# Optimization experiments

Hardware: AMD Instinct MI355X
Metric: run time of the kernel (lower is better)

The kernel has to match this reference:

```python
import jax, jax.numpy as jnp
import numpy as np

D_MODEL = 512
N_LAYERS = 6
N_HEADS = 8
INNER = 2048
VOCAB = 2048
SEQ = 128
BATCH = 256
HEAD_DIM = D_MODEL // N_HEADS
EPS = 1e-5


def _pos_encoding(seq_len, d_model):
    pos = jnp.arange(seq_len, dtype=jnp.float32)[:, None]          # [S,1]
    i = jnp.arange(d_model // 2, dtype=jnp.float32)[None, :]       # [1,d/2]
    theta = pos / jnp.power(10000.0, 2.0 * i / d_model)            # [S,d/2]
    # interleave sin at even indices, cos at odd indices
    return jnp.stack([jnp.sin(theta), jnp.cos(theta)], axis=-1).reshape(seq_len, d_model)


def _layer_norm_2d(x):
    # F.layer_norm(x, (N, dims)): normalize over last TWO dims, no affine
    m = jnp.mean(x, axis=(1, 2), keepdims=True)
    v = jnp.mean(jnp.square(x - m), axis=(1, 2), keepdims=True)
    return (x - m) / jnp.sqrt(v + EPS)


def setup_inputs() -> dict:
    key = jax.random.key(0)
    ks = jax.random.split(key, 12)
    s = 0.02
    x = jax.random.randint(ks[0], (BATCH, SEQ), 0, VOCAB)
    emb = jax.random.normal(ks[1], (VOCAB, D_MODEL), jnp.float32) * s
    Wq = jax.random.normal(ks[2], (N_LAYERS, N_HEADS, D_MODEL, HEAD_DIM), jnp.float32) * s
    bq = jax.random.normal(ks[3], (N_LAYERS, N_HEADS, HEAD_DIM), jnp.float32) * s
    Wk = jax.random.normal(ks[4], (N_LAYERS, N_HEADS, D_MODEL, HEAD_DIM), jnp.float32) * s
    bk = jax.random.normal(ks[5], (N_LAYERS, N_HEADS, HEAD_DIM), jnp.float32) * s
    Wv = jax.random.normal(ks[6], (N_LAYERS, N_HEADS, D_MODEL, HEAD_DIM), jnp.float32) * s
    bv = jax.random.normal(ks[7], (N_LAYERS, N_HEADS, HEAD_DIM), jnp.float32) * s
    W1 = jax.random.normal(ks[8], (N_LAYERS, D_MODEL, INNER), jnp.float32) * s
    b1 = jax.random.normal(ks[9], (N_LAYERS, INNER), jnp.float32) * s
    W2 = jax.random.normal(ks[10], (N_LAYERS, INNER, D_MODEL), jnp.float32) * s
    b2 = jax.random.normal(ks[11], (N_LAYERS, D_MODEL), jnp.float32) * s
    return {"x": x, "emb": emb, "Wq": Wq, "bq": bq, "Wk": Wk, "bk": bk,
            "Wv": Wv, "bv": bv, "W1": W1, "b1": b1, "W2": W2, "b2": b2}


def reference(x, emb, Wq, bq, Wk, bk, Wv, bv, W1, b1, W2, b2):
    B, S = x.shape
    pe = _pos_encoding(SEQ, D_MODEL)
    h = emb[x] + pe[None, :, :]                                     # [B,S,D]
    scale = HEAD_DIM ** -0.5
    for l in range(N_LAYERS):
        q = jnp.einsum('bsd,hde->bhse', h, Wq[l]) + bq[l][None, :, None, :]
        k = jnp.einsum('bsd,hde->bhse', h, Wk[l]) + bk[l][None, :, None, :]
        v = jnp.einsum('bsd,hde->bhse', h, Wv[l]) + bv[l][None, :, None, :]
        scores = jnp.einsum('bhse,bhte->bhst', q, k) * scale        # no softmax!
        attn = jnp.einsum('bhst,bhte->bhse', scores, v)             # [B,H,S,E]
        attn = jnp.transpose(attn, (0, 2, 1, 3)).reshape(B, S, D_MODEL)
        h = _layer_norm_2d(h + attn)
        ff = jax.nn.relu(h @ W1[l] + b1[l]) @ W2[l] + b2[l]
        h = _layer_norm_2d(h + ff)
    return h
```

## Files before the change

kernel.cpp:

```cpp
#include <hip/hip_runtime.h>
#include <stdint.h>

#define NLAYERS 6
#define DMODEL  512
#define NHEADS  8
#define HDIM    64
#define INNER   2048
#define SEQ     128
#define BATCH   256
#define NTOK    (BATCH*SEQ)

typedef __attribute__((ext_vector_type(4))) float f32x4;
typedef __attribute__((ext_vector_type(8))) _Float16 hfrag;

typedef const __attribute__((address_space(1))) void* gas1p;
typedef __attribute__((address_space(3))) void* las3p;

__device__ __forceinline__ void load_lds16(const void* g, void* l) {
  __builtin_amdgcn_global_load_lds((gas1p)(uintptr_t)g, (las3p)(uint32_t)(uintptr_t)l, 16, 0, 0);
}

__device__ __forceinline__ ushort f2h(float f) {
  return __builtin_bit_cast(ushort, (_Float16)f);
}
__device__ __forceinline__ float h2f(ushort u) {
  return (float)__builtin_bit_cast(_Float16, u);
}

__device__ __forceinline__ f32x4 mfma16(hfrag a, hfrag b, f32x4 c) {
  return __builtin_amdgcn_mfma_f32_16x16x32_f16(a, b, c, 0, 0, 0);
}


__global__ void prep_qkv(const float* __restrict__ Wq, const float* __restrict__ Wk,
                         const float* __restrict__ Wv, const float* __restrict__ bq,
                         const float* __restrict__ bk, const float* __restrict__ bv,
                         ushort* __restrict__ Wt, float* __restrict__ biasq) {
  int idx = blockIdx.x*256 + threadIdx.x;
  if (idx >= NLAYERS*1536*512) return;
  const int k = idx & 511;
  const int n = (idx >> 9) % 1536;
  const int l = idx / (1536*512);
  const int which = n >> 9, hh = (n >> 6) & 7, e = n & 63;
  const float* W = (which == 0) ? Wq : ((which == 1) ? Wk : Wv);
  Wt[idx] = f2h(W[(((size_t)l*NHEADS + hh)*DMODEL + k)*HDIM + e]);
  if (k == 0) {
    const float* bb = (which == 0) ? bq : ((which == 1) ? bk : bv);
    biasq[l*1536 + n] = bb[((size_t)l*NHEADS + hh)*HDIM + e];
  }
}

__global__ void prep_w1(const float* __restrict__ W1, ushort* __restrict__ W1t) {
  int idx = blockIdx.x*256 + threadIdx.x;
  if (idx >= NLAYERS*INNER*512) return;
  const int k = idx & 511;
  const int n = (idx >> 9) % INNER;
  const int l = idx / (INNER*512);
  W1t[idx] = f2h(W1[((size_t)l*DMODEL + k)*INNER + n]);
}

__global__ void prep_w2(const float* __restrict__ W2, ushort* __restrict__ W2t) {
  int idx = blockIdx.x*256 + threadIdx.x;
  if (idx >= NLAYERS*512*INNER) return;
  const int k = idx & 2047;
  const int n = (idx >> 11) & 511;
  const int l = idx / (512*INNER);
  W2t[idx] = f2h(W2[((size_t)l*INNER + k)*DMODEL + n]);
}


__global__ void embed_kernel(const int* __restrict__ x, const float* __restrict__ emb,
                             ushort* __restrict__ hb) {
  const int t = blockIdx.x;
  const int i = threadIdx.x;
  const int s = t & (SEQ-1);
  const int tok = x[t];
  const float freq = expf(-(float)i * (9.210340371976184f / 256.0f));
  const float th = (float)s * freq;
  const float sn = sinf(th), cs = cosf(th);
  const size_t base = (size_t)t*DMODEL;
  const float v0 = emb[(size_t)tok*DMODEL + 2*i]     + sn;
  const float v1 = emb[(size_t)tok*DMODEL + 2*i + 1] + cs;
  *(uint*)(hb + base + 2*i) = (uint)f2h(v0) | ((uint)f2h(v1) << 16);
}


template<int K, int EPI>
__global__ __launch_bounds__(256, 2) void gemm_t(
    const ushort* __restrict__ A, const ushort* __restrict__ Bt,
    const float* __restrict__ bias, ushort* __restrict__ outb,
    const int ldc, const int nbn) {
  __shared__ __align__(16) char lds[73728];
  constexpr int NKT = K / 32;
  const int t = threadIdx.x;
  const int lane = t & 63, wc = t >> 6;
  const int cpx = (int)gridDim.x >> 3;
  const int wg  = ((int)blockIdx.x & 7) * cpx + ((int)blockIdx.x >> 3);
  const int bm = wg / nbn, bn = wg % nbn;

  const int fr = lane & 15;
  const int cxor = (((lane >> 4) ^ ((fr >> 1) & 3)) << 4);

  float bias_r[4];
  #pragma unroll
  for (int n = 0; n < 4; ++n) bias_r[n] = bias[bn*256 + wc*64 + n*16 + fr];
  asm volatile("" : "+v"(bias_r[0]), "+v"(bias_r[1]), "+v"(bias_r[2]), "+v"(bias_r[3]));

  const int srow = t >> 2;
  const int scc  = (t & 3) ^ ((t >> 3) & 3);
  const ushort* aSrc = A  + ((size_t)bm*128 + srow)*K + scc*8;
  const ushort* bSrc = Bt + ((size_t)bn*256 + srow)*K + scc*8;

  auto stage_t = [&](int j, int slot) {
    char* dst = lds + slot*24576 + t*16;
    const ushort* as = aSrc + j*32;
    load_lds16(as,                  dst);
    load_lds16(as + (size_t)64*K,   dst + 4096);
    const ushort* bs = bSrc + j*32;
    #pragma unroll
    for (int i = 0; i < 4; ++i)
      load_lds16(bs + (size_t)(i*64)*K, dst + 8192 + i*4096);
  };

  f32x4 acc[8][4] = {};

  stage_t(0, 0); stage_t(1, 1);
  asm volatile("s_waitcnt vmcnt(6)" ::: "memory");
  __builtin_amdgcn_s_barrier();

  int rs = 0, ss = 2;
  #pragma unroll 1
  for (int kt = 0; kt < NKT; ++kt) {
    const char* sl = lds + rs*24576;
    hfrag a[8], b[4];
    #pragma unroll
    for (int m = 0; m < 8; ++m)
      a[m] = *(const hfrag*)(sl + (m*16 + fr)*64 + cxor);
    #pragma unroll
    for (int n = 0; n < 4; ++n)
      b[n] = *(const hfrag*)(sl + 8192 + (wc*64 + n*16 + fr)*64 + cxor);
    if (kt + 2 < NKT) stage_t(kt + 2, ss);
    __builtin_amdgcn_s_setprio(1);
    #pragma unroll
    for (int m = 0; m < 8; ++m)
      #pragma unroll
      for (int n = 0; n < 4; ++n)
        acc[m][n] = mfma16(a[m], b[n], acc[m][n]);
    __builtin_amdgcn_s_setprio(0);
    if (kt + 2 < NKT) {
      asm volatile("s_waitcnt vmcnt(6)" ::: "memory");
    } else if (kt + 2 == NKT) {
      asm volatile("s_waitcnt vmcnt(0)" ::: "memory");
    }
    if (kt + 1 < NKT) __builtin_amdgcn_s_barrier();
    rs = (rs == 2) ? 0 : rs + 1;
    ss = (ss == 2) ? 0 : ss + 1;
  }

  #pragma unroll
  for (int m = 0; m < 8; ++m) {
    __syncthreads();
    #pragma unroll
    for (int n = 0; n < 4; ++n) {
      const int cc16 = wc*4 + n;
      #pragma unroll
      for (int r4 = 0; r4 < 4; ++r4) {
        const int row = ((lane >> 4) << 2) + r4;
        float v = acc[m][n][r4] + bias_r[n];
        if constexpr (EPI == 1) v = fmaxf(v, 0.0f);
        *(ushort*)(lds + row*512 + ((cc16 ^ (row >> 2)) << 5) + fr*2) = f2h(v);
      }
    }
    __syncthreads();
    const int er = t >> 4;
    ushort* gp = outb + (size_t)(bm*128 + m*16 + er)*ldc + bn*256;
    #pragma unroll
    for (int p = 0; p < 2; ++p) {
      const int cj = (t & 15) + p*16;
      const uint4 v = *(const uint4*)(lds + er*512 + (((cj >> 1) ^ (er >> 2)) << 5) + ((cj & 1) << 4));
      *(uint4*)(gp + cj*8) = v;
    }
  }
}


__global__ __launch_bounds__(512, 1) void attn_ln(
    const ushort* __restrict__ qkv, ushort* __restrict__ hb) {
  __shared__ __align__(16) char lds[131072];
  __shared__ float red_[8], redq_[8], stat_[2];
  const int t = threadIdx.x;
  const int w = t >> 6, lane = t & 63;
  const int b = blockIdx.x, h = w;
  const int fr = lane & 15;
  const ushort* tokbase = qkv + (size_t)b*SEQ*1536;
  ushort* wl  = (ushort*)(lds + w*16384);
  ushort* kch = wl;
  ushort* vch = wl + 2048;

  f32x4 acc1[4][4] = {};
  #pragma unroll 1
  for (int sb = 0; sb < 4; ++sb) {
    const int s0 = sb*32;
    const int sr = lane >> 1;
    #pragma unroll
    for (int i = 0; i < 4; ++i) {
      const int cc  = i*2 + (lane & 1);
      const int ccs = cc ^ (sr & 7);
      const ushort* g = tokbase + (size_t)(s0+sr)*1536 + h*64 + cc*8;
      *(uint4*)(kch + sr*64 + ccs*8) = *(const uint4*)(g + 512);
      *(uint4*)(vch + sr*64 + ccs*8) = *(const uint4*)(g + 1024);
    }
    hfrag ak[4], av[4];
    #pragma unroll
    for (int m = 0; m < 4; ++m) {
      const int e1 = m*16 + (lane & 15);
      const int ccb = e1 >> 3, el = e1 & 7;
      #pragma unroll
      for (int j = 0; j < 8; ++j) {
        const int s = (lane >> 4)*8 + j;
        ak[m][j] = __builtin_bit_cast(_Float16, kch[s*64 + ((ccb ^ (s & 7))*8) + el]);
        av[m][j] = __builtin_bit_cast(_Float16, vch[s*64 + ((ccb ^ (s & 7))*8) + el]);
      }
    }
    #pragma unroll
    for (int m = 0; m < 4; ++m)
      #pragma unroll
      for (int n = 0; n < 4; ++n)
        acc1[m][n] = mfma16(ak[m], av[n], acc1[m][n]);
  }

  ushort* tv = wl;
  #pragma unroll
  for (int m = 0; m < 4; ++m)
    #pragma unroll
    for (int n = 0; n < 4; ++n)
      #pragma unroll
      for (int r4 = 0; r4 < 4; ++r4) {
        const int e1 = m*16 + (lane >> 4)*4 + r4;
        const int e2 = n*16 + (lane & 15);
        tv[e2*72 + e1] = f2h(acc1[m][n][r4] * 0.125f);
      }

  f32x4 acc2[8][4] = {};
  #pragma unroll
  for (int eb = 0; eb < 2; ++eb) {
    const int e1b = eb*32 + (lane >> 4)*8;
    hfrag aq[8], bk2[4];
    #pragma unroll
    for (int m = 0; m < 8; ++m) {
      const int s = m*16 + (lane & 15);
      aq[m] = *(const hfrag*)(tokbase + (size_t)s*1536 + h*64 + e1b);
    }
    #pragma unroll
    for (int n = 0; n < 4; ++n) {
      const int e2 = n*16 + (lane & 15);
      bk2[n] = *(const hfrag*)(tv + e2*72 + e1b);
    }
    #pragma unroll
    for (int m = 0; m < 8; ++m)
      #pragma unroll
      for (int n = 0; n < 4; ++n)
        acc2[m][n] = mfma16(aq[m], bk2[n], acc2[m][n]);
  }

  __syncthreads();
  #pragma unroll
  for (int m = 0; m < 8; ++m)
    #pragma unroll
    for (int n = 0; n < 4; ++n)
      #pragma unroll
      for (int r4 = 0; r4 < 4; ++r4) {
        const int row = m*16 + ((lane >> 4) << 2) + r4;
        const int ch  = (w*4 + n) ^ ((row >> 2) & 3) ^ (w >> 1);
        *(ushort*)(lds + row*1024 + ch*32 + fr*2) = f2h(acc2[m][n][r4]);
      }
  __syncthreads();

  const int r = t >> 2, qd = t & 3;
  const ushort* hrow = hb + ((size_t)b*SEQ + r)*DMODEL + qd*128;
  uint4 vc[16];
  float s = 0.f, q2 = 0.f;
  #pragma unroll
  for (int j = 0; j < 8; ++j) {
    const int ch = (qd*8 + j) ^ ((r >> 2) & 3) ^ qd;
    const uint4 d0 = *(const uint4*)(lds + r*1024 + ch*32);
    const uint4 d1 = *(const uint4*)(lds + r*1024 + ch*32 + 16);
    const uint4 h0 = *(const uint4*)(hrow + j*16);
    const uint4 h1 = *(const uint4*)(hrow + j*16 + 8);
    uint4 v0, v1;
    #pragma unroll
    for (int c = 0; c < 4; ++c) {
      float a0 = h2f((ushort)((&h0.x)[c] & 0xffffu)) + h2f((ushort)((&d0.x)[c] & 0xffffu));
      float a1 = h2f((ushort)((&h0.x)[c] >> 16))     + h2f((ushort)((&d0.x)[c] >> 16));
      float b0 = h2f((ushort)((&h1.x)[c] & 0xffffu)) + h2f((ushort)((&d1.x)[c] & 0xffffu));
      float b1 = h2f((ushort)((&h1.x)[c] >> 16))     + h2f((ushort)((&d1.x)[c] >> 16));
      s += a0 + a1 + b0 + b1;
      q2 += a0*a0 + a1*a1 + b0*b0 + b1*b1;
      (&v0.x)[c] = (uint)f2h(a0) | ((uint)f2h(a1) << 16);
      (&v1.x)[c] = (uint)f2h(b0) | ((uint)f2h(b1) << 16);
    }
    vc[2*j] = v0; vc[2*j+1] = v1;
  }
  #pragma unroll
  for (int off = 32; off > 0; off >>= 1) {
    s  += __shfl_down(s, off);
    q2 += __shfl_down(q2, off);
  }
  if (lane == 0) { red_[w] = s; redq_[w] = q2; }
  __syncthreads();
  if (t == 0) {
    float S = 0.f, Q = 0.f;
    #pragma unroll
    for (int i = 0; i < 8; ++i) { S += red_[i]; Q += redq_[i]; }
    const float mean = S * (1.0f/65536.0f);
    stat_[0] = mean;
    stat_[1] = rsqrtf(Q * (1.0f/65536.0f) - mean*mean + 1e-5f);
  }
  __syncthreads();
  const float mean = stat_[0], rstd = stat_[1];
  ushort* orow = hb + ((size_t)b*SEQ + r)*DMODEL + qd*128;
  #pragma unroll
  for (int j = 0; j < 16; ++j) {
    const uint4 u = vc[j];
    uint4 o;
    #pragma unroll
    for (int c = 0; c < 4; ++c) {
      const float o0 = (h2f((ushort)((&u.x)[c] & 0xffffu)) - mean) * rstd;
      const float o1 = (h2f((ushort)((&u.x)[c] >> 16))     - mean) * rstd;
      (&o.x)[c] = (uint)f2h(o0) | ((uint)f2h(o1) << 16);
    }
    *(uint4*)(orow + j*8) = o;
  }
}


template<bool FINAL>
__global__ __launch_bounds__(512, 1) void gemm_f(
    const ushort* __restrict__ A, const ushort* __restrict__ Bt,
    const float* __restrict__ bias, ushort* __restrict__ hb, float* __restrict__ hf) {
  __shared__ __align__(16) char lds[131072];
  __shared__ float red_[8], redq_[8], stat_[2];
  constexpr int K = 2048, NKT = 64;
  const int t = threadIdx.x;
  const int lane = t & 63, w = t >> 6;
  const int bm = blockIdx.x;
  const int fr = lane & 15;
  const int cxor = (((lane >> 4) ^ ((fr >> 1) & 3)) << 4);

  float bias_r[4];
  #pragma unroll
  for (int n = 0; n < 4; ++n) bias_r[n] = bias[w*64 + n*16 + fr];
  asm volatile("" : "+v"(bias_r[0]), "+v"(bias_r[1]), "+v"(bias_r[2]), "+v"(bias_r[3]));

  const int srow = t >> 2;
  const int scc  = (t & 3) ^ ((t >> 3) & 3);
  const ushort* aSrc = A  + ((size_t)bm*128 + srow)*K + scc*8;
  const ushort* bSrc = Bt + (size_t)srow*K + scc*8;

  auto stage = [&](int j, int slot) {
    char* dst = lds + slot*40960 + t*16;
    load_lds16(aSrc + j*32, dst);
    #pragma unroll
    for (int i = 0; i < 4; ++i)
      load_lds16(bSrc + (size_t)(i*128)*K + j*32, dst + 8192 + i*8192);
  };

  f32x4 acc[8][4] = {};

  stage(0, 0); stage(1, 1);
  asm volatile("s_waitcnt vmcnt(5)" ::: "memory");
  __builtin_amdgcn_s_barrier();

  int rs = 0, ss = 2;
  #pragma unroll 1
  for (int kt = 0; kt < NKT; ++kt) {
    const char* sl = lds + rs*40960;
    hfrag a[8], b[4];
    #pragma unroll
    for (int m = 0; m < 8; ++m)
      a[m] = *(const hfrag*)(sl + (m*16 + fr)*64 + cxor);
    #pragma unroll
    for (int n = 0; n < 4; ++n)
      b[n] = *(const hfrag*)(sl + 8192 + (w*64 + n*16 + fr)*64 + cxor);
    if (kt + 2 < NKT) stage(kt + 2, ss);
    __builtin_amdgcn_s_setprio(1);
    #pragma unroll
    for (int m = 0; m < 8; ++m)
      #pragma unroll
      for (int n = 0; n < 4; ++n)
        acc[m][n] = mfma16(a[m], b[n], acc[m][n]);
    __builtin_amdgcn_s_setprio(0);
    if (kt + 2 < NKT) {
      asm volatile("s_waitcnt vmcnt(5)" ::: "memory");
    } else if (kt + 2 == NKT) {
      asm volatile("s_waitcnt vmcnt(0)" ::: "memory");
    }
    if (kt + 1 < NKT) __builtin_amdgcn_s_barrier();
    rs = (rs == 2) ? 0 : rs + 1;
    ss = (ss == 2) ? 0 : ss + 1;
  }

  __syncthreads();
  #pragma unroll
  for (int m = 0; m < 8; ++m)
    #pragma unroll
    for (int n = 0; n < 4; ++n)
      #pragma unroll
      for (int r4 = 0; r4 < 4; ++r4) {
        const int row = m*16 + ((lane >> 4) << 2) + r4;
        const int ch  = (w*4 + n) ^ ((row >> 2) & 3) ^ (w >> 1);
        *(ushort*)(lds + row*1024 + ch*32 + fr*2) = f2h(acc[m][n][r4] + bias_r[n]);
      }
  __syncthreads();

  const int r = t >> 2, qd = t & 3;
  const ushort* hrow = hb + ((size_t)bm*SEQ + r)*DMODEL + qd*128;
  uint4 vc[16];
  float s = 0.f, q2 = 0.f;
  #pragma unroll
  for (int j = 0; j < 8; ++j) {
    const int ch = (qd*8 + j) ^ ((r >> 2) & 3) ^ qd;
    const uint4 d0 = *(const uint4*)(lds + r*1024 + ch*32);
    const uint4 d1 = *(const uint4*)(lds + r*1024 + ch*32 + 16);
    const uint4 h0 = *(const uint4*)(hrow + j*16);
    const uint4 h1 = *(const uint4*)(hrow + j*16 + 8);
    uint4 v0, v1;
    #pragma unroll
    for (int c = 0; c < 4; ++c) {
      float a0 = h2f((ushort)((&h0.x)[c] & 0xffffu)) + h2f((ushort)((&d0.x)[c] & 0xffffu));
      float a1 = h2f((ushort)((&h0.x)[c] >> 16))     + h2f((ushort)((&d0.x)[c] >> 16));
      float b0 = h2f((ushort)((&h1.x)[c] & 0xffffu)) + h2f((ushort)((&d1.x)[c] & 0xffffu));
      float b1 = h2f((ushort)((&h1.x)[c] >> 16))     + h2f((ushort)((&d1.x)[c] >> 16));
      s += a0 + a1 + b0 + b1;
      q2 += a0*a0 + a1*a1 + b0*b0 + b1*b1;
      (&v0.x)[c] = (uint)f2h(a0) | ((uint)f2h(a1) << 16);
      (&v1.x)[c] = (uint)f2h(b0) | ((uint)f2h(b1) << 16);
    }
    vc[2*j] = v0; vc[2*j+1] = v1;
  }
  #pragma unroll
  for (int off = 32; off > 0; off >>= 1) {
    s  += __shfl_down(s, off);
    q2 += __shfl_down(q2, off);
  }
  if (lane == 0) { red_[w] = s; redq_[w] = q2; }
  __syncthreads();
  if (t == 0) {
    float S = 0.f, Q = 0.f;
    #pragma unroll
    for (int i = 0; i < 8; ++i) { S += red_[i]; Q += redq_[i]; }
    const float mean = S * (1.0f/65536.0f);
    stat_[0] = mean;
    stat_[1] = rsqrtf(Q * (1.0f/65536.0f) - mean*mean + 1e-5f);
  }
  __syncthreads();
  const float mean = stat_[0], rstd = stat_[1];
  if constexpr (FINAL) {
    float* frow = hf + ((size_t)bm*SEQ + r)*DMODEL + qd*128;
    #pragma unroll
    for (int j = 0; j < 16; ++j) {
      const uint4 u = vc[j];
      f32x4 o0, o1;
      #pragma unroll
      for (int c = 0; c < 2; ++c) {
        o0[2*c]   = (h2f((ushort)((&u.x)[c] & 0xffffu)) - mean) * rstd;
        o0[2*c+1] = (h2f((ushort)((&u.x)[c] >> 16))     - mean) * rstd;
        o1[2*c]   = (h2f((ushort)((&u.x)[c+2] & 0xffffu)) - mean) * rstd;
        o1[2*c+1] = (h2f((ushort)((&u.x)[c+2] >> 16))     - mean) * rstd;
      }
      *(f32x4*)(frow + j*8)     = o0;
      *(f32x4*)(frow + j*8 + 4) = o1;
    }
  } else {
    ushort* orow = hb + ((size_t)bm*SEQ + r)*DMODEL + qd*128;
    #pragma unroll
    for (int j = 0; j < 16; ++j) {
      const uint4 u = vc[j];
      uint4 o;
      #pragma unroll
      for (int c = 0; c < 4; ++c) {
        const float o0 = (h2f((ushort)((&u.x)[c] & 0xffffu)) - mean) * rstd;
        const float o1 = (h2f((ushort)((&u.x)[c] >> 16))     - mean) * rstd;
        (&o.x)[c] = (uint)f2h(o0) | ((uint)f2h(o1) << 16);
      }
      *(uint4*)(orow + j*8) = o;
    }
  }
}


extern "C" void kernel_launch(void* const* d_in, const int* in_sizes, int n_in,
                              void* d_out, int out_size, void* d_ws, size_t ws_size,
                              hipStream_t stream) {
  const int*   x   = (const int*)d_in[0];
  const float* emb = (const float*)d_in[1];
  const float* Wq  = (const float*)d_in[2];
  const float* bq  = (const float*)d_in[3];
  const float* Wk  = (const float*)d_in[4];
  const float* bk  = (const float*)d_in[5];
  const float* Wv  = (const float*)d_in[6];
  const float* bv  = (const float*)d_in[7];
  const float* W1  = (const float*)d_in[8];
  const float* b1  = (const float*)d_in[9];
  const float* W2  = (const float*)d_in[10];
  const float* b2  = (const float*)d_in[11];
  float* h = (float*)d_out;

  char* p = (char*)d_ws;
  size_t off = 0;
  auto alloc = [&](size_t bytes) { char* r = p + off; off += (bytes + 255) & ~(size_t)255; return r; };
  ushort* Wqkv_t = (ushort*)alloc((size_t)NLAYERS*1536*512*2);
  ushort* W1t    = (ushort*)alloc((size_t)NLAYERS*INNER*512*2);
  ushort* W2t    = (ushort*)alloc((size_t)NLAYERS*512*INNER*2);
  float*  biasq  = (float*)alloc((size_t)NLAYERS*1536*4);
  ushort* hbf    = (ushort*)alloc((size_t)NTOK*512*2);
  ushort* big    = (ushort*)alloc((size_t)NTOK*2048*2);

  prep_qkv<<<(NLAYERS*1536*512 + 255)/256, 256, 0, stream>>>(Wq, Wk, Wv, bq, bk, bv, Wqkv_t, biasq);
  prep_w1<<<(NLAYERS*INNER*512 + 255)/256, 256, 0, stream>>>(W1, W1t);
  prep_w2<<<(NLAYERS*512*INNER + 255)/256, 256, 0, stream>>>(W2, W2t);
  embed_kernel<<<NTOK, 256, 0, stream>>>(x, emb, hbf);

  for (int l = 0; l < NLAYERS; ++l) {
    gemm_t<512,0><<<1536, 256, 0, stream>>>(
        hbf, Wqkv_t + (size_t)l*1536*512, biasq + (size_t)l*1536, big, 1536, 6);
    attn_ln<<<BATCH, 512, 0, stream>>>(big, hbf);
    gemm_t<512,1><<<2048, 256, 0, stream>>>(
        hbf, W1t + (size_t)l*INNER*512, b1 + (size_t)l*INNER, big, 2048, 8);
    if (l == NLAYERS-1) {
      gemm_f<true><<<BATCH, 512, 0, stream>>>(
          big, W2t + (size_t)l*512*INNER, b2 + (size_t)l*512, hbf, h);
    } else {
      gemm_f<false><<<BATCH, 512, 0, stream>>>(
          big, W2t + (size_t)l*512*INNER, b2 + (size_t)l*512, hbf, nullptr);
    }
  }
}
```

Measured before the change: 1.664 ms.

## Enlarge GEMM tile to 256x256 with 8 waves and double buffering

After: 1.714 ms. 1.03x slower.

```diff
diff --git a/kernel.cpp b/kernel.cpp
--- a/kernel.cpp
+++ b/kernel.cpp
@@ -86,14 +86,15 @@
 
 
 template<int K, int EPI>
-__global__ __launch_bounds__(256, 2) void gemm_t(
+__global__ __launch_bounds__(512, 2) void gemm_2(
     const ushort* __restrict__ A, const ushort* __restrict__ Bt,
     const float* __restrict__ bias, ushort* __restrict__ outb,
     const int ldc, const int nbn) {
-  __shared__ __align__(16) char lds[73728];
+  __shared__ __align__(16) char lds[65536];
   constexpr int NKT = K / 32;
   const int t = threadIdx.x;
-  const int lane = t & 63, wc = t >> 6;
+  const int lane = t & 63, w = t >> 6;
+  const int wr = w >> 2, wc = w & 3;
   const int cpx = (int)gridDim.x >> 3;
   const int wg  = ((int)blockIdx.x & 7) * cpx + ((int)blockIdx.x >> 3);
   const int bm = wg / nbn, bn = wg % nbn;
@@ -108,38 +109,34 @@
 
   const int srow = t >> 2;
   const int scc  = (t & 3) ^ ((t >> 3) & 3);
-  const ushort* aSrc = A  + ((size_t)bm*128 + srow)*K + scc*8;
+  const ushort* aSrc = A  + ((size_t)bm*256 + srow)*K + scc*8;
   const ushort* bSrc = Bt + ((size_t)bn*256 + srow)*K + scc*8;
 
-  auto stage_t = [&](int j, int slot) {
-    char* dst = lds + slot*24576 + t*16;
-    const ushort* as = aSrc + j*32;
-    load_lds16(as,                  dst);
-    load_lds16(as + (size_t)64*K,   dst + 4096);
-    const ushort* bs = bSrc + j*32;
-    #pragma unroll
-    for (int i = 0; i < 4; ++i)
-      load_lds16(bs + (size_t)(i*64)*K, dst + 8192 + i*4096);
+  auto stage = [&](int j, int slot) {
+    char* dst = lds + slot*32768 + t*16;
+    load_lds16(aSrc + j*32,                 dst);
+    load_lds16(aSrc + (size_t)128*K + j*32, dst + 8192);
+    load_lds16(bSrc + j*32,                 dst + 16384);
+    load_lds16(bSrc + (size_t)128*K + j*32, dst + 24576);
   };
 
   f32x4 acc[8][4] = {};
 
-  stage_t(0, 0); stage_t(1, 1);
-  asm volatile("s_waitcnt vmcnt(6)" ::: "memory");
+  stage(0, 0);
+  asm volatile("s_waitcnt vmcnt(0)" ::: "memory");
   __builtin_amdgcn_s_barrier();
 
-  int rs = 0, ss = 2;
   #pragma unroll 1
   for (int kt = 0; kt < NKT; ++kt) {
-    const char* sl = lds + rs*24576;
+    if (kt + 1 < NKT) stage(kt + 1, (kt + 1) & 1);
+    const char* sl = lds + (kt & 1)*32768;
     hfrag a[8], b[4];
     #pragma unroll
     for (int m = 0; m < 8; ++m)
-      a[m] = *(const hfrag*)(sl + (m*16 + fr)*64 + cxor);
+      a[m] = *(const hfrag*)(sl + (wr*128 + m*16 + fr)*64 + cxor);
     #pragma unroll
     for (int n = 0; n < 4; ++n)
-      b[n] = *(const hfrag*)(sl + 8192 + (wc*64 + n*16 + fr)*64 + cxor);
-    if (kt + 2 < NKT) stage_t(kt + 2, ss);
+      b[n] = *(const hfrag*)(sl + 16384 + (wc*64 + n*16 + fr)*64 + cxor);
     __builtin_amdgcn_s_setprio(1);
     #pragma unroll
     for (int m = 0; m < 8; ++m)
@@ -147,38 +144,43 @@
       for (int n = 0; n < 4; ++n)
         acc[m][n] = mfma16(a[m], b[n], acc[m][n]);
     __builtin_amdgcn_s_setprio(0);
-    if (kt + 2 < NKT) {
-      asm volatile("s_waitcnt vmcnt(6)" ::: "memory");
-    } else if (kt + 2 == NKT) {
+    if (kt + 1 < NKT) {
       asm volatile("s_waitcnt vmcnt(0)" ::: "memory");
-    }
-    if (kt + 1 < NKT) __builtin_amdgcn_s_barrier();
-    rs = (rs == 2) ? 0 : rs + 1;
-    ss = (ss == 2) ? 0 : ss + 1;
-  }
-
-  #pragma unroll
-  for (int m = 0; m < 8; ++m) {
+      __builtin_amdgcn_s_barrier();
+    }
+  }
+
+  #pragma unroll
+  for (int mm = 0; mm < 4; ++mm) {
     __syncthreads();
     #pragma unroll
-    for (int n = 0; n < 4; ++n) {
-      const int cc16 = wc*4 + n;
-      #pragma unroll
-      for (int r4 = 0; r4 < 4; ++r4) {
-        const int row = ((lane >> 4) << 2) + r4;
-        float v = acc[m][n][r4] + bias_r[n];
-        if constexpr (EPI == 1) v = fmaxf(v, 0.0f);
-        *(ushort*)(lds + row*512 + ((cc16 ^ (row >> 2)) << 5) + fr*2) = f2h(v);
+    for (int mi = 0; mi < 2; ++mi) {
+      const int m = mm*2 + mi;
+      #pragma unroll
+      for (int n = 0; n < 4; ++n) {
+        const int cc16 = wc*4 + n;
+        #pragma unroll
+        for (int r4 = 0; r4 < 4; ++r4) {
+          const int rr = ((lane >> 4) << 2) + r4;
+          const int lr = wr*32 + mi*16 + rr;
+          float v = acc[m][n][r4] + bias_r[n];
+          if constexpr (EPI == 1) v = fmaxf(v, 0.0f);
+          *(ushort*)(lds + lr*512 + ((cc16 ^ (rr >> 2)) << 5) + fr*2) = f2h(v);
+        }
       }
     }
     __syncthreads();
-    const int er = t >> 4;
-    ushort* gp = outb + (size_t)(bm*128 + m*16 + er)*ldc + bn*256;
-    #pragma unroll
-    for (int p = 0; p < 2; ++p) {
-      const int cj = (t & 15) + p*16;
-      const uint4 v = *(const uint4*)(lds + er*512 + (((cj >> 1) ^ (er >> 2)) << 5) + ((cj & 1) << 4));
-      *(uint4*)(gp + cj*8) = v;
+    #pragma unroll
+    for (int pr = 0; pr < 2; ++pr) {
+      const int lr = (t >> 4) + pr*32;
+      const int grow = bm*256 + (lr >> 5)*128 + mm*32 + (lr & 31);
+      ushort* gp = outb + (size_t)grow*ldc + bn*256;
+      #pragma unroll
+      for (int pc = 0; pc < 2; ++pc) {
+        const int cj = (t & 15) + pc*16;
+        const uint4 v = *(const uint4*)(lds + lr*512 + (((cj >> 1) ^ ((lr & 15) >> 2)) << 5) + ((cj & 1) << 4));
+        *(uint4*)(gp + cj*8) = v;
+      }
     }
   }
 }
@@ -522,10 +524,10 @@
   embed_kernel<<<NTOK, 256, 0, stream>>>(x, emb, hbf);
 
   for (int l = 0; l < NLAYERS; ++l) {
-    gemm_t<512,0><<<1536, 256, 0, stream>>>(
+    gemm_2<512,0><<<768, 512, 0, stream>>>(
         hbf, Wqkv_t + (size_t)l*1536*512, biasq + (size_t)l*1536, big, 1536, 6);
     attn_ln<<<BATCH, 512, 0, stream>>>(big, hbf);
-    gemm_t<512,1><<<2048, 256, 0, stream>>>(
+    gemm_2<512,1><<<1024, 512, 0, stream>>>(
         hbf, W1t + (size_t)l*INNER*512, b1 + (size_t)l*INNER, big, 2048, 8);
     if (l == NLAYERS-1) {
       gemm_f<true><<<BATCH, 512, 0, stream>>>(
```
